# Optimization experiments

Measured on AMD Instinct MI355X. Metric: run time of the kernel, lower is better.

The kernel has to match this reference:

```python
import jax, jax.numpy as jnp
import numpy as np

# dims (match init_kwargs / input_specs)
B, T, IN, H, OUT, BR = 128, 250, 700, 512, 20, 4
VTH, DT, WARMUP = 1.0, 1.0, 10


@jax.custom_vjp
def spike_fn(v):
    # Heaviside spike with surrogate gradient (ActFun_adp style)
    return (v > 0.0).astype(v.dtype)

def _spike_fwd(v):
    return spike_fn(v), v

def _spike_bwd(v, g):
    gamma, lens = 0.5, 0.5  # gaussian surrogate
    return (g * gamma * jnp.exp(-v * v / (2.0 * lens * lens)),)

spike_fn.defvjp(_spike_fwd, _spike_bwd)


def make_mask(rng, out_dim, in_dim, branch):
    # each output neuron's branch j sees a disjoint random slice of inputs
    m = np.zeros((out_dim * branch, in_dim), np.float32)
    seg = in_dim // branch
    for i in range(out_dim):
        perm = rng.permutation(in_dim)
        for j in range(branch):
            m[i * branch + j, perm[j * seg:(j + 1) * seg]] = 1.0
    return jnp.asarray(m)


def setup_inputs() -> dict:
    key = jax.random.key(0)
    ks = jax.random.split(key, 12)
    rng = np.random.default_rng(0)
    lim1 = 1.0 / np.sqrt(IN)
    lim2 = 1.0 / np.sqrt(H)
    return {
        "x": jax.random.uniform(ks[0], (B, T, IN), dtype=jnp.float32),
        "W1": jax.random.uniform(ks[1], (H * BR, IN), minval=-lim1, maxval=lim1),
        "b1": jax.random.uniform(ks[2], (H * BR,), minval=-lim1, maxval=lim1),
        "tau_m1": jax.random.uniform(ks[3], (H,), minval=0.0, maxval=4.0),
        "tau_n1": jax.random.uniform(ks[4], (H, BR), minval=0.0, maxval=4.0),
        "mask1": make_mask(rng, H, IN, BR),
        "W2": jax.random.uniform(ks[5], (H * BR, H), minval=-lim2, maxval=lim2),
        "b2": jax.random.uniform(ks[6], (H * BR,), minval=-lim2, maxval=lim2),
        "tau_m2": jax.random.uniform(ks[7], (H,), minval=0.0, maxval=4.0),
        "tau_n2": jax.random.uniform(ks[8], (H, BR), minval=0.0, maxval=4.0),
        "mask2": make_mask(rng, H, H, BR),
        "Wo": jax.random.uniform(ks[9], (OUT, H), minval=-lim2, maxval=lim2),
        "bo": jax.random.uniform(ks[10], (OUT,), minval=-lim2, maxval=lim2),
        "tau_mo": jax.random.uniform(ks[11], (OUT,), minval=0.0, maxval=4.0),
    }


def reference(x, W1, b1, tau_m1, tau_n1, mask1, W2, b2, tau_m2, tau_n2, mask2, Wo, bo, tau_mo):
    beta1 = jax.nn.sigmoid(tau_n1)   # [H,BR] dendritic decay
    alpha1 = jax.nn.sigmoid(tau_m1)  # [H]   membrane decay
    beta2 = jax.nn.sigmoid(tau_n2)
    alpha2 = jax.nn.sigmoid(tau_m2)
    alpha_o = jax.nn.sigmoid(tau_mo)  # [OUT]
    Wm1 = W1 * mask1  # dendritic branch connectivity mask
    Wm2 = W2 * mask2
    Bsz = x.shape[0]
    Hd, Br = tau_n1.shape
    Od = tau_mo.shape[0]

    init = (jnp.zeros((Bsz, Hd, Br)), jnp.zeros((Bsz, Hd)), jnp.zeros((Bsz, Hd)),
            jnp.zeros((Bsz, Hd, Br)), jnp.zeros((Bsz, Hd)), jnp.zeros((Bsz, Hd)),
            jnp.zeros((Bsz, Od)))

    def step(c, xt):
        d1, m1, s1, d2, m2, s2, mo = c
        # layer 1: dendritic filter then LIF membrane with soft reset
        d1 = beta1 * d1 + (1.0 - beta1) * (xt @ Wm1.T + b1).reshape(Bsz, Hd, Br)
        m1 = m1 * alpha1 + (1.0 - alpha1) * DT * d1.sum(-1) - VTH * s1
        s1 = spike_fn(m1 - VTH)
        # layer 2
        d2 = beta2 * d2 + (1.0 - beta2) * (s1 @ Wm2.T + b2).reshape(Bsz, Hd, Br)
        m2 = m2 * alpha2 + (1.0 - alpha2) * DT * d2.sum(-1) - VTH * s2
        s2 = spike_fn(m2 - VTH)
        # leaky readout integrator (no spiking)
        mo = mo * alpha_o + (1.0 - alpha_o) * DT * (s2 @ Wo.T + bo)
        return (d1, m1, s1, d2, m2, s2, mo), jax.nn.softmax(mo, axis=1)

    _, ys = jax.lax.scan(step, init, jnp.swapaxes(x, 0, 1))  # ys: [T,B,OUT]
    # readout_mode == 'sum_softmax': skip steps i <= warmup_steps, sum the rest
    return ys[WARMUP + 1:].sum(0)
```

## Files before the change

kernel.cpp:

```cpp
#include <hip/hip_runtime.h>
#include <math.h>
#include <stdint.h>

#define B_    128
#define T_    250
#define IN_   700
#define INP_  704
#define H_    512
#define OUT_  20
#define BR_   4
#define HB_   2048
#define WARM_ 10
#define VTH_  1.0f

typedef __attribute__((ext_vector_type(8)))  _Float16 half8;
typedef __attribute__((ext_vector_type(4)))  float f32x4;
typedef __attribute__((ext_vector_type(16))) float f32x16;
typedef __attribute__((ext_vector_type(4)))  int i32x4;
typedef __attribute__((ext_vector_type(16))) int i32x16;
typedef const __attribute__((address_space(1))) void* gptr_t;
typedef __attribute__((address_space(3))) void* lptr_t;

__global__ __launch_bounds__(256)
void w1prep_kernel(const float* __restrict__ W, const float* __restrict__ M,
                   _Float16* __restrict__ w0, _Float16* __restrict__ w1) {
    int i = blockIdx.x * 256 + threadIdx.x;
    if (i >= HB_ * INP_) return;
    int r = i / INP_, c = i - r * INP_;
    float v = (c < IN_) ? W[(size_t)r * IN_ + c] * M[(size_t)r * IN_ + c] : 0.f;
    _Float16 h0 = (_Float16)v;
    w0[i] = h0;
    w1[i] = (_Float16)(v - (float)h0);
}

__global__ __launch_bounds__(256)
void w2prep_kernel(const float* __restrict__ W, const float* __restrict__ M,
                   int8_t* __restrict__ p2, int8_t* __restrict__ p1,
                   int8_t* __restrict__ p0) {
    int i = blockIdx.x * 256 + threadIdx.x;
    if (i >= HB_ * H_) return;
    float v = W[i] * M[i];
    int q = (int)lrintf(v * 67108864.f);
    int b0 = (int)(int8_t)(q & 0xFF);  q = (q - b0) >> 8;
    int b1 = (int)(int8_t)(q & 0xFF);  int b2 = (q - b1) >> 8;
    p0[i] = (int8_t)b0; p1[i] = (int8_t)b1; p2[i] = (int8_t)b2;
}

__global__ __launch_bounds__(256)
void woprep_kernel(const float* __restrict__ Wo, _Float16* __restrict__ wo0,
                   _Float16* __restrict__ wo1) {
    int i = blockIdx.x * 256 + threadIdx.x;
    if (i >= 32 * H_) return;
    int n = i >> 9;
    float v = (n < OUT_) ? Wo[(size_t)n * H_ + (i & (H_ - 1))] : 0.f;
    _Float16 h0 = (_Float16)v;
    wo0[i] = h0;
    wo1[i] = (_Float16)(v - (float)h0);
}

__global__ __launch_bounds__(256)
void convx_kernel(const float* __restrict__ x, _Float16* __restrict__ x0,
                  _Float16* __restrict__ x1, int t0, int tc, int ntot) {
    int i = blockIdx.x * 256 + threadIdx.x;
    if (i >= ntot) return;
    int r = i / INP_, c = i - r * INP_;
    int bb = r / tc, tl = r - bb * tc;
    float v = (c < IN_) ? x[((size_t)bb * T_ + t0 + tl) * IN_ + c] : 0.f;
    _Float16 h0 = (_Float16)v;
    x0[i] = h0;
    x1[i] = (_Float16)(v - (float)h0);
}

__global__ void zero_kernel(float* __restrict__ p, int n4) {
    int i = blockIdx.x * blockDim.x + threadIdx.x;
    if (i < n4) ((float4*)p)[i] = make_float4(0.f, 0.f, 0.f, 0.f);
}

__global__ __launch_bounds__(256)
void l1_gemm_kernel(const _Float16* __restrict__ x0, const _Float16* __restrict__ x1,
                    const _Float16* __restrict__ w0, const _Float16* __restrict__ w1,
                    const float* __restrict__ bias, float* __restrict__ C) {
    __shared__ alignas(16) _Float16 S[2 * 16384];
    const int tid  = threadIdx.x;
    const int wave = tid >> 6, lane = tid & 63;
    const int bm = blockIdx.y * 128, bn = blockIdx.x * 128;

    const int    srow  = tid >> 2;
    const int    skoff = (((tid & 3) ^ ((srow >> 1) & 3)) * 8);
    const size_t aoff0 = (size_t)(bm + srow) * INP_ + skoff;
    const size_t aoff1 = aoff0 + (size_t)64 * INP_;
    const size_t boff0 = (size_t)(bn + srow) * INP_ + skoff;
    const size_t boff1 = boff0 + (size_t)64 * INP_;
    const int lo = wave * 512;

    const int wm = wave & 1, wn = wave >> 1;
    const int row = lane & 31;
    const int khq = lane >> 5;
    const int key = (lane >> 1) & 3;
    const int cK0 = ((0 + khq) ^ key) * 8;
    const int cK1 = ((2 + khq) ^ key) * 8;

    f32x16 acc[2][2] = {};

    auto stage = [&](int kt, int base) {
        const int k0 = kt * 32;
        _Float16* Sb = S + base;
        __builtin_amdgcn_global_load_lds((gptr_t)(x0 + aoff0 + k0), (lptr_t)(Sb + lo),          16, 0, 0);
        __builtin_amdgcn_global_load_lds((gptr_t)(x0 + aoff1 + k0), (lptr_t)(Sb + 2048  + lo),  16, 0, 0);
        __builtin_amdgcn_global_load_lds((gptr_t)(x1 + aoff0 + k0), (lptr_t)(Sb + 4096  + lo),  16, 0, 0);
        __builtin_amdgcn_global_load_lds((gptr_t)(x1 + aoff1 + k0), (lptr_t)(Sb + 6144  + lo),  16, 0, 0);
        __builtin_amdgcn_global_load_lds((gptr_t)(w0 + boff0 + k0), (lptr_t)(Sb + 8192  + lo),  16, 0, 0);
        __builtin_amdgcn_global_load_lds((gptr_t)(w0 + boff1 + k0), (lptr_t)(Sb + 10240 + lo),  16, 0, 0);
        __builtin_amdgcn_global_load_lds((gptr_t)(w1 + boff0 + k0), (lptr_t)(Sb + 12288 + lo),  16, 0, 0);
        __builtin_amdgcn_global_load_lds((gptr_t)(w1 + boff1 + k0), (lptr_t)(Sb + 14336 + lo),  16, 0, 0);
    };

    auto compute = [&](int base) {
        const _Float16* A0b = S + base;
        const _Float16* A1b = A0b + 4096;
        const _Float16* B0b = A0b + 8192;
        const _Float16* B1b = A0b + 12288;
        half8 a0f[2][2], a1f[2][2], b0f[2][2], b1f[2][2];
#pragma unroll
        for (int mt = 0; mt < 2; mt++) {
            const _Float16* ar = &A0b[(wm * 64 + mt * 32 + row) * 32];
            a0f[mt][0] = *(const half8*)&ar[cK0];
            a0f[mt][1] = *(const half8*)&ar[cK1];
        }
#pragma unroll
        for (int nt = 0; nt < 2; nt++) {
            const _Float16* br = &B0b[(wn * 64 + nt * 32 + row) * 32];
            b0f[nt][0] = *(const half8*)&br[cK0];
            b0f[nt][1] = *(const half8*)&br[cK1];
        }
        __builtin_amdgcn_s_setprio(1);
#pragma unroll
        for (int ks = 0; ks < 2; ks++)
#pragma unroll
            for (int mt = 0; mt < 2; mt++)
#pragma unroll
                for (int nt = 0; nt < 2; nt++)
                    acc[mt][nt] = __builtin_amdgcn_mfma_f32_32x32x16_f16(
                        a0f[mt][ks], b0f[nt][ks], acc[mt][nt], 0, 0, 0);
        __builtin_amdgcn_s_setprio(0);
#pragma unroll
        for (int nt = 0; nt < 2; nt++) {
            const _Float16* br = &B1b[(wn * 64 + nt * 32 + row) * 32];
            b1f[nt][0] = *(const half8*)&br[cK0];
            b1f[nt][1] = *(const half8*)&br[cK1];
        }
        __builtin_amdgcn_s_setprio(1);
#pragma unroll
        for (int ks = 0; ks < 2; ks++)
#pragma unroll
            for (int mt = 0; mt < 2; mt++)
#pragma unroll
                for (int nt = 0; nt < 2; nt++)
                    acc[mt][nt] = __builtin_amdgcn_mfma_f32_32x32x16_f16(
                        a0f[mt][ks], b1f[nt][ks], acc[mt][nt], 0, 0, 0);
        __builtin_amdgcn_s_setprio(0);
#pragma unroll
        for (int mt = 0; mt < 2; mt++) {
            const _Float16* ar = &A1b[(wm * 64 + mt * 32 + row) * 32];
            a1f[mt][0] = *(const half8*)&ar[cK0];
            a1f[mt][1] = *(const half8*)&ar[cK1];
        }
        __builtin_amdgcn_s_setprio(1);
#pragma unroll
        for (int ks = 0; ks < 2; ks++)
#pragma unroll
            for (int mt = 0; mt < 2; mt++)
#pragma unroll
                for (int nt = 0; nt < 2; nt++)
                    acc[mt][nt] = __builtin_amdgcn_mfma_f32_32x32x16_f16(
                        a1f[mt][ks], b0f[nt][ks], acc[mt][nt], 0, 0, 0);
        __builtin_amdgcn_s_setprio(0);
    };

    stage(0, 0);
    asm volatile("s_waitcnt vmcnt(0)" ::: "memory");
    __builtin_amdgcn_s_barrier();

    int cur = 0;
    for (int kt = 0; kt < INP_ / 32 - 1; kt++) {
        const int base = cur * 16384;
        stage(kt + 1, base ^ 16384);
        compute(base);
        asm volatile("s_waitcnt vmcnt(0) lgkmcnt(0)" ::: "memory");
        __builtin_amdgcn_s_barrier();
        cur ^= 1;
    }
    compute(cur * 16384);

    const int col = lane & 31;
    const int rb  = 4 * (lane >> 5);
#pragma unroll
    for (int nt = 0; nt < 2; nt++) {
        const int gc = bn + wn * 64 + nt * 32 + col;
        const float bv = bias[gc];
#pragma unroll
        for (int mt = 0; mt < 2; mt++) {
#pragma unroll
            for (int reg = 0; reg < 16; reg++) {
                const int gr = bm + wm * 64 + mt * 32 + (reg & 3) + 8 * (reg >> 2) + rb;
                C[(size_t)gr * HB_ + gc] = acc[mt][nt][reg] + bv;
            }
        }
    }
}

__global__ __launch_bounds__(256)
void mfma_i8_gemm_kernel(const int8_t* __restrict__ A,
                         const int8_t* __restrict__ p2, const int8_t* __restrict__ p1,
                         const int8_t* __restrict__ p0,
                         const float* __restrict__ bias, float* __restrict__ C) {
    __shared__ alignas(16) int8_t S[2 * 16384];
    const int tid  = threadIdx.x;
    const int wave = tid >> 6, lane = tid & 63;
    const int bm = blockIdx.y * 128, bn = blockIdx.x * 128;

    const int    srow  = tid >> 2;
    const int    skoff = (((tid & 3) ^ ((srow >> 1) & 3)) * 16);
    const size_t aoff0 = (size_t)(bm + srow) * H_ + skoff;
    const size_t aoff1 = aoff0 + (size_t)64 * H_;
    const size_t boff0 = (size_t)(bn + srow) * H_ + skoff;
    const size_t boff1 = boff0 + (size_t)64 * H_;
    const int lo = wave * 1024;

    const int wm = wave & 1, wn = wave >> 1;
    const int row = lane & 31;
    const int khq = lane >> 5;
    const int key = (lane >> 1) & 3;
    const int cK0 = ((0 + khq) ^ key) * 16;
    const int cK1 = ((2 + khq) ^ key) * 16;

    i32x16 acc[2][2] = {};

    auto stage = [&](int i, int base) {
        const int s  = i >> 3;
        const int k0 = (i & 7) * 64;
        const int8_t* pw = (s == 0) ? p2 : (s == 1) ? p1 : p0;
        int8_t* Sb = S + base;
        __builtin_amdgcn_global_load_lds((gptr_t)(A  + aoff0 + k0), (lptr_t)(Sb + lo),          16, 0, 0);
        __builtin_amdgcn_global_load_lds((gptr_t)(A  + aoff1 + k0), (lptr_t)(Sb + 4096  + lo),  16, 0, 0);
        __builtin_amdgcn_global_load_lds((gptr_t)(pw + boff0 + k0), (lptr_t)(Sb + 8192  + lo),  16, 0, 0);
        __builtin_amdgcn_global_load_lds((gptr_t)(pw + boff1 + k0), (lptr_t)(Sb + 12288 + lo),  16, 0, 0);
    };

    auto compute = [&](int base) {
        const int8_t* Ab = S + base;
        const int8_t* Bb = Ab + 8192;
        i32x4 af[2][2], bf[2][2];
#pragma unroll
        for (int mt = 0; mt < 2; mt++) {
            const int8_t* ar = &Ab[(wm * 64 + mt * 32 + row) * 64];
            af[mt][0] = *(const i32x4*)&ar[cK0];
            af[mt][1] = *(const i32x4*)&ar[cK1];
        }
#pragma unroll
        for (int nt = 0; nt < 2; nt++) {
            const int8_t* br = &Bb[(wn * 64 + nt * 32 + row) * 64];
            bf[nt][0] = *(const i32x4*)&br[cK0];
            bf[nt][1] = *(const i32x4*)&br[cK1];
        }
        __builtin_amdgcn_s_setprio(1);
#pragma unroll
        for (int ks = 0; ks < 2; ks++)
#pragma unroll
            for (int mt = 0; mt < 2; mt++)
#pragma unroll
                for (int nt = 0; nt < 2; nt++)
                    acc[mt][nt] = __builtin_amdgcn_mfma_i32_32x32x32_i8(
                        af[mt][ks], bf[nt][ks], acc[mt][nt], 0, 0, 0);
        __builtin_amdgcn_s_setprio(0);
    };

    stage(0, 0);
    asm volatile("s_waitcnt vmcnt(0)" ::: "memory");
    __builtin_amdgcn_s_barrier();

    int cur = 0;
    for (int i = 0; i < 23; i++) {
        const int base = cur * 16384;
        stage(i + 1, base ^ 16384);
        if (i == 8 || i == 16) {
#pragma unroll
            for (int mt = 0; mt < 2; mt++)
#pragma unroll
                for (int nt = 0; nt < 2; nt++) acc[mt][nt] *= 256;
        }
        compute(base);
        asm volatile("s_waitcnt vmcnt(0) lgkmcnt(0)" ::: "memory");
        __builtin_amdgcn_s_barrier();
        cur ^= 1;
    }
    compute(cur * 16384);

    const float scale = 1.f / 67108864.f;
    const int col = lane & 31;
    const int rb  = 4 * (lane >> 5);
#pragma unroll
    for (int nt = 0; nt < 2; nt++) {
        const int gc = bn + wn * 64 + nt * 32 + col;
        const float bv = bias[gc];
#pragma unroll
        for (int mt = 0; mt < 2; mt++) {
#pragma unroll
            for (int reg = 0; reg < 16; reg++) {
                const int gr = bm + wm * 64 + mt * 32 + (reg & 3) + 8 * (reg >> 2) + rb;
                C[(size_t)gr * HB_ + gc] = (float)acc[mt][nt][reg] * scale + bv;
            }
        }
    }
}

#define SCAN_BODY(SPIKE_STORE)                                                  \
    int idx = blockIdx.x * 256 + threadIdx.x;                                   \
    int b = idx >> 9;                                                           \
    int h = idx & (H_ - 1);                                                     \
    float alpha = 1.f / (1.f + expf(-tau_m[h]));                                \
    float4 tn = ((const float4*)tau_n)[h];                                      \
    float4 beta;                                                                \
    beta.x = 1.f / (1.f + expf(-tn.x));                                         \
    beta.y = 1.f / (1.f + expf(-tn.y));                                         \
    beta.z = 1.f / (1.f + expf(-tn.z));                                         \
    beta.w = 1.f / (1.f + expf(-tn.w));                                         \
    float4 d = ((const float4*)dst)[idx];                                       \
    float m = mst[idx];                                                         \
    float sp = spst[idx];                                                       \
    const float* cp = cur + (size_t)b * tc * HB_ + h * BR_;                     \
    for (int t = 0; t < tc; t++) {                                              \
        float4 c = *(const float4*)cp;                                          \
        cp += HB_;                                                              \
        d.x = beta.x * d.x + (1.f - beta.x) * c.x;                              \
        d.y = beta.y * d.y + (1.f - beta.y) * c.y;                              \
        d.z = beta.z * d.z + (1.f - beta.z) * c.z;                              \
        d.w = beta.w * d.w + (1.f - beta.w) * c.w;                              \
        float s4 = ((d.x + d.y) + d.z) + d.w;                                   \
        m = m * alpha + (1.f - alpha) * s4 - VTH_ * sp;                         \
        sp = (m > VTH_) ? 1.f : 0.f;                                            \
        SPIKE_STORE;                                                            \
    }                                                                           \
    ((float4*)dst)[idx] = d;                                                    \
    mst[idx] = m;                                                               \
    spst[idx] = sp;

__global__ __launch_bounds__(256)
void scan_i8_kernel(const float* __restrict__ cur, float* __restrict__ dst,
                    float* __restrict__ mst, float* __restrict__ spst,
                    int8_t* __restrict__ sout, const float* __restrict__ tau_m,
                    const float* __restrict__ tau_n, int tc) {
    SCAN_BODY(sout[((size_t)b * tc + t) * H_ + h] = (int8_t)(m > VTH_))
}

__global__ __launch_bounds__(256)
void scan_f16_kernel(const float* __restrict__ cur, float* __restrict__ dst,
                     float* __restrict__ mst, float* __restrict__ spst,
                     _Float16* __restrict__ sout, const float* __restrict__ tau_m,
                     const float* __restrict__ tau_n, int tc) {
    SCAN_BODY(sout[((size_t)b * tc + t) * H_ + h] = (_Float16)sp)
}

__global__ __launch_bounds__(256)
void rdot_mfma_kernel(const _Float16* __restrict__ s2c, const _Float16* __restrict__ wo0,
                      const _Float16* __restrict__ wo1, const float* __restrict__ bo,
                      float* __restrict__ curo, int t0, int tc) {
    __shared__ alignas(16) _Float16 S[2 * 6144];
    const int tid  = threadIdx.x;
    const int wave = tid >> 6, lane = tid & 63;
    const int bm = blockIdx.x * 128;

    const int    srow  = tid >> 2;
    const int    skoff = (((tid & 3) ^ ((srow >> 1) & 3)) * 8);
    const size_t aoff0 = (size_t)(bm + srow) * H_ + skoff;
    const size_t aoff1 = aoff0 + (size_t)64 * H_;
    const _Float16* bsrc = (wave < 2) ? wo0 : wo1;
    const int bw = wave & 1;
    const size_t boff = (size_t)(bw * 16 + (lane >> 2)) * H_
                      + ((lane & 3) ^ ((lane >> 3) & 3)) * 8;
    const int loA = wave * 512;
    const int loB = 4096 + (wave >> 1) * 1024 + bw * 512;

    const int fr = lane & 15;
    const int key = (lane >> 1) & 3;
    const int cK  = (((lane >> 4) ^ key) * 8);

    f32x4 acc[2][2] = {};

    auto stage = [&](int kt, int base) {
        const int k0 = kt * 32;
        _Float16* Sb = S + base;
        __builtin_amdgcn_global_load_lds((gptr_t)(s2c + aoff0 + k0),  (lptr_t)(Sb + loA),        16, 0, 0);
        __builtin_amdgcn_global_load_lds((gptr_t)(s2c + aoff1 + k0),  (lptr_t)(Sb + 2048 + loA), 16, 0, 0);
        __builtin_amdgcn_global_load_lds((gptr_t)(bsrc + boff + k0),  (lptr_t)(Sb + loB),        16, 0, 0);
    };

    auto compute = [&](int base) {
        const _Float16* Ab  = S + base;
        const _Float16* B0b = Ab + 4096;
        const _Float16* B1b = Ab + 5120;
        half8 af[2], b0[2], b1[2];
#pragma unroll
        for (int mi = 0; mi < 2; mi++)
            af[mi] = *(const half8*)&Ab[(wave * 32 + mi * 16 + fr) * 32 + cK];
#pragma unroll
        for (int ni = 0; ni < 2; ni++) {
            b0[ni] = *(const half8*)&B0b[(ni * 16 + fr) * 32 + cK];
            b1[ni] = *(const half8*)&B1b[(ni * 16 + fr) * 32 + cK];
        }
        __builtin_amdgcn_s_setprio(1);
#pragma unroll
        for (int mi = 0; mi < 2; mi++)
#pragma unroll
            for (int ni = 0; ni < 2; ni++) {
                acc[mi][ni] = __builtin_amdgcn_mfma_f32_16x16x32_f16(af[mi], b0[ni], acc[mi][ni], 0, 0, 0);
                acc[mi][ni] = __builtin_amdgcn_mfma_f32_16x16x32_f16(af[mi], b1[ni], acc[mi][ni], 0, 0, 0);
            }
        __builtin_amdgcn_s_setprio(0);
    };

    stage(0, 0);
    asm volatile("s_waitcnt vmcnt(0)" ::: "memory");
    __builtin_amdgcn_s_barrier();

    int cur = 0;
    for (int kt = 0; kt < H_ / 32 - 1; kt++) {
        const int base = cur * 6144;
        stage(kt + 1, base ^ 6144);
        compute(base);
        asm volatile("s_waitcnt vmcnt(0) lgkmcnt(0)" ::: "memory");
        __builtin_amdgcn_s_barrier();
        cur ^= 1;
    }
    compute(cur * 6144);

    const int cc = lane & 15;
    const int cr = (lane >> 4) * 4;
#pragma unroll
    for (int ni = 0; ni < 2; ni++) {
        const int gc = ni * 16 + cc;
        if (gc < OUT_) {
            const float bv = bo[gc];
#pragma unroll
            for (int mi = 0; mi < 2; mi++) {
#pragma unroll
                for (int r = 0; r < 4; r++) {
                    const int gr = bm + wave * 32 + mi * 16 + cr + r;
                    const int bb = gr / tc, tl = gr - bb * tc;
                    curo[((size_t)bb * T_ + t0 + tl) * OUT_ + gc] = acc[mi][ni][r] + bv;
                }
            }
        }
    }
}

#define RT_SEG 12
#define RT_LEN 21

__global__ __launch_bounds__(256)
void readout_kernel(const float* __restrict__ curo, const float* __restrict__ tau_mo,
                    float* __restrict__ out) {
    __shared__ float moS[T_ * OUT_];
    __shared__ float segA[RT_SEG][OUT_];
    __shared__ float segU[RT_SEG][OUT_];
    __shared__ float pre[RT_SEG][OUT_];
    __shared__ float accS[OUT_];
    const int b = blockIdx.x;
    const int tid = threadIdx.x;
    const float* cb = curo + (size_t)b * T_ * OUT_;

    const int o = tid % OUT_;
    const int sg = tid / OUT_;
    const float ao = 1.f / (1.f + expf(-tau_mo[o]));

    if (tid < RT_SEG * OUT_) {
        int t0 = sg * RT_LEN;
        int t1 = min(T_, t0 + RT_LEN);
        float u = 0.f, Ap = 1.f;
        for (int t = t0; t < t1; t++) {
            u = ao * u + (1.f - ao) * cb[t * OUT_ + o];
            Ap *= ao;
        }
        segU[sg][o] = u; segA[sg][o] = Ap;
    }
    if (tid < OUT_) accS[tid] = 0.f;
    __syncthreads();
    if (tid < OUT_) {
        float m = 0.f;
        for (int s = 0; s < RT_SEG; s++) {
            pre[s][tid] = m;
            m = segA[s][tid] * m + segU[s][tid];
        }
    }
    __syncthreads();
    if (tid < RT_SEG * OUT_) {
        int t0 = sg * RT_LEN;
        int t1 = min(T_, t0 + RT_LEN);
        float m = pre[sg][o];
        for (int t = t0; t < t1; t++) {
            m = ao * m + (1.f - ao) * cb[t * OUT_ + o];
            moS[t * OUT_ + o] = m;
        }
    }
    __syncthreads();
    if (tid >= WARM_ + 1 && tid < T_) {
        int t = tid;
        float mx = -3.0e38f;
#pragma unroll
        for (int o2 = 0; o2 < OUT_; o2++) mx = fmaxf(mx, moS[t * OUT_ + o2]);
        float es[OUT_]; float se = 0.f;
#pragma unroll
        for (int o2 = 0; o2 < OUT_; o2++) {
            float e = expf(moS[t * OUT_ + o2] - mx);
            es[o2] = e; se += e;
        }
        float inv = 1.f / se;
#pragma unroll
        for (int o2 = 0; o2 < OUT_; o2++) atomicAdd(&accS[o2], es[o2] * inv);
    }
    __syncthreads();
    if (tid < OUT_) out[(size_t)b * OUT_ + tid] = accS[tid];
}

extern "C" void kernel_launch(void* const* d_in, const int* in_sizes, int n_in,
                              void* d_out, int out_size, void* d_ws, size_t ws_size,
                              hipStream_t stream) {
    const float* x      = (const float*)d_in[0];
    const float* W1     = (const float*)d_in[1];
    const float* b1     = (const float*)d_in[2];
    const float* tau_m1 = (const float*)d_in[3];
    const float* tau_n1 = (const float*)d_in[4];
    const float* mask1  = (const float*)d_in[5];
    const float* W2     = (const float*)d_in[6];
    const float* b2     = (const float*)d_in[7];
    const float* tau_m2 = (const float*)d_in[8];
    const float* tau_n2 = (const float*)d_in[9];
    const float* mask2  = (const float*)d_in[10];
    const float* Wo     = (const float*)d_in[11];
    const float* bo     = (const float*)d_in[12];
    const float* tau_mo = (const float*)d_in[13];
    float* out = (float*)d_out;

    int ncs;  int tcs[3];
    bool single = (ws_size >= (size_t)368000000);
    if (single)                                { ncs = 1; tcs[0] = 250; }
    else if (ws_size >= (size_t)219000000)     { ncs = 2; tcs[0] = tcs[1] = 125; }
    else                                       { ncs = 3; tcs[0] = 100; tcs[1] = 100; tcs[2] = 50; }
    const int tcm = tcs[0];

    char* p = (char*)d_ws;
    auto alloc = [&](size_t bytes) { char* r = p; p += (bytes + 255) & ~(size_t)255; return r; };
    _Float16* w10 = (_Float16*)alloc((size_t)HB_ * INP_ * 2);
    _Float16* w11 = (_Float16*)alloc((size_t)HB_ * INP_ * 2);
    int8_t*   q2  = (int8_t*)alloc((size_t)HB_ * H_);
    int8_t*   q1  = (int8_t*)alloc((size_t)HB_ * H_);
    int8_t*   q0  = (int8_t*)alloc((size_t)HB_ * H_);
    _Float16* wo0 = (_Float16*)alloc((size_t)32 * H_ * 2);
    _Float16* wo1 = (_Float16*)alloc((size_t)32 * H_ * 2);
    _Float16* xc0 = (_Float16*)alloc((size_t)B_ * tcm * INP_ * 2);
    _Float16* xc1 = (_Float16*)alloc((size_t)B_ * tcm * INP_ * 2);
    int8_t*   s1c;
    _Float16* s2c;
    if (single) {
        s1c = (int8_t*)xc0;
        s2c = (_Float16*)xc1;
    } else {
        s1c = (int8_t*)alloc((size_t)B_ * tcm * H_);
        s2c = (_Float16*)alloc((size_t)B_ * tcm * H_ * 2);
    }
    float* cur    = (float*)alloc((size_t)B_ * tcm * HB_ * 4);
    float* curo   = (float*)alloc((size_t)B_ * T_ * OUT_ * 4);
    float* st     = (float*)alloc((size_t)786432 * 4);
    float* d1  = st;
    float* m1  = d1 + (size_t)B_ * H_ * BR_;
    float* sp1 = m1 + (size_t)B_ * H_;
    float* d2  = sp1 + (size_t)B_ * H_;
    float* m2  = d2 + (size_t)B_ * H_ * BR_;
    float* sp2 = m2 + (size_t)B_ * H_;

    w1prep_kernel<<<(HB_ * INP_ + 255) / 256, 256, 0, stream>>>(W1, mask1, w10, w11);
    w2prep_kernel<<<(HB_ * H_ + 255) / 256, 256, 0, stream>>>(W2, mask2, q2, q1, q0);
    woprep_kernel<<<(32 * H_ + 255) / 256, 256, 0, stream>>>(Wo, wo0, wo1);
    zero_kernel<<<(786432 / 4 + 255) / 256, 256, 0, stream>>>(st, 786432 / 4);

    int t0 = 0;
    for (int c = 0; c < ncs; c++) {
        const int tc = tcs[c];
        const int M = B_ * tc;
        dim3 gg(HB_ / 128, M / 128);
        convx_kernel<<<(M * INP_ + 255) / 256, 256, 0, stream>>>(x, xc0, xc1, t0, tc, M * INP_);
        l1_gemm_kernel<<<gg, 256, 0, stream>>>(xc0, xc1, w10, w11, b1, cur);
        scan_i8_kernel<<<B_ * H_ / 256, 256, 0, stream>>>(cur, d1, m1, sp1, s1c, tau_m1, tau_n1, tc);
        mfma_i8_gemm_kernel<<<gg, 256, 0, stream>>>(s1c, q2, q1, q0, b2, cur);
        scan_f16_kernel<<<B_ * H_ / 256, 256, 0, stream>>>(cur, d2, m2, sp2, s2c, tau_m2, tau_n2, tc);
        rdot_mfma_kernel<<<M / 128, 256, 0, stream>>>(s2c, wo0, wo1, bo, curo, t0, tc);
        t0 += tc;
    }
    readout_kernel<<<B_, 256, 0, stream>>>(curo, tau_mo, out);
}
```

Baseline: 827.7 us.

## Load A operands directly to registers from pre-tiled x layout, remap workgroups

The x conversion kernel now writes x0/x1 in an MFMA-fragment-tiled layout, so the layer-1 GEMM can load A fragments straight from global memory into registers instead of staging them through LDS. LDS is halved to hold only the B (weight) tiles, and the k-loop is unrolled by two with register double-buffering and sched barriers, using partial vmcnt waits. Workgroup IDs are also remapped in an XCD-aware way. This cuts LDS traffic and footprint but adds register pressure, and it depends on other users of x0/x1 expecting the new layout.

```diff
diff --git a/kernel.cpp b/kernel.cpp
--- a/kernel.cpp
+++ b/kernel.cpp
@@ -21,6 +21,8 @@
 typedef const __attribute__((address_space(1))) void* gptr_t;
 typedef __attribute__((address_space(3))) void* lptr_t;
 
+#define SB0() __builtin_amdgcn_sched_barrier(0)
+
 __global__ __launch_bounds__(256)
 void w1prep_kernel(const float* __restrict__ W, const float* __restrict__ M,
                    _Float16* __restrict__ w0, _Float16* __restrict__ w1) {
@@ -67,8 +69,10 @@
     int bb = r / tc, tl = r - bb * tc;
     float v = (c < IN_) ? x[((size_t)bb * T_ + t0 + tl) * IN_ + c] : 0.f;
     _Float16 h0 = (_Float16)v;
-    x0[i] = h0;
-    x1[i] = (_Float16)(v - (float)h0);
+    size_t off = ((((size_t)(r >> 5) * 22 + (c >> 5)) * 4 + ((c >> 3) & 3)) * 32
+                  + (r & 31)) * 8 + (c & 7);
+    x0[off] = h0;
+    x1[off] = (_Float16)(v - (float)h0);
 }
 
 __global__ void zero_kernel(float* __restrict__ p, int n4) {
@@ -80,15 +84,18 @@
 void l1_gemm_kernel(const _Float16* __restrict__ x0, const _Float16* __restrict__ x1,
                     const _Float16* __restrict__ w0, const _Float16* __restrict__ w1,
                     const float* __restrict__ bias, float* __restrict__ C) {
-    __shared__ alignas(16) _Float16 S[2 * 16384];
+    __shared__ alignas(16) _Float16 S[2 * 8192];
     const int tid  = threadIdx.x;
     const int wave = tid >> 6, lane = tid & 63;
-    const int bm = blockIdx.y * 128, bn = blockIdx.x * 128;
+
+    const int nwg = (int)(gridDim.x * gridDim.y);
+    const int cpx = nwg >> 3;
+    const int id0 = (int)(blockIdx.y * gridDim.x + blockIdx.x);
+    const int id  = (id0 & 7) * cpx + (id0 >> 3);
+    const int bm = (id >> 4) * 128, bn = (id & 15) * 128;
 
     const int    srow  = tid >> 2;
     const int    skoff = (((tid & 3) ^ ((srow >> 1) & 3)) * 8);
-    const size_t aoff0 = (size_t)(bm + srow) * INP_ + skoff;
-    const size_t aoff1 = aoff0 + (size_t)64 * INP_;
     const size_t boff0 = (size_t)(bn + srow) * INP_ + skoff;
     const size_t boff1 = boff0 + (size_t)64 * INP_;
     const int lo = wave * 512;
@@ -100,38 +107,45 @@
     const int cK0 = ((0 + khq) ^ key) * 8;
     const int cK1 = ((2 + khq) ^ key) * 8;
 
+    const size_t mb0   = (size_t)(bm >> 5) + wm * 2;
+    const size_t aoffl = (size_t)(lane >> 5) * 256 + (size_t)(lane & 31) * 8;
+
     f32x16 acc[2][2] = {};
-
-    auto stage = [&](int kt, int base) {
+    half8 aP[2][2][2], aQ[2][2][2];
+
+    auto stageB = [&](int kt, int base) {
         const int k0 = kt * 32;
         _Float16* Sb = S + base;
-        __builtin_amdgcn_global_load_lds((gptr_t)(x0 + aoff0 + k0), (lptr_t)(Sb + lo),          16, 0, 0);
-        __builtin_amdgcn_global_load_lds((gptr_t)(x0 + aoff1 + k0), (lptr_t)(Sb + 2048  + lo),  16, 0, 0);
-        __builtin_amdgcn_global_load_lds((gptr_t)(x1 + aoff0 + k0), (lptr_t)(Sb + 4096  + lo),  16, 0, 0);
-        __builtin_amdgcn_global_load_lds((gptr_t)(x1 + aoff1 + k0), (lptr_t)(Sb + 6144  + lo),  16, 0, 0);
-        __builtin_amdgcn_global_load_lds((gptr_t)(w0 + boff0 + k0), (lptr_t)(Sb + 8192  + lo),  16, 0, 0);
-        __builtin_amdgcn_global_load_lds((gptr_t)(w0 + boff1 + k0), (lptr_t)(Sb + 10240 + lo),  16, 0, 0);
-        __builtin_amdgcn_global_load_lds((gptr_t)(w1 + boff0 + k0), (lptr_t)(Sb + 12288 + lo),  16, 0, 0);
-        __builtin_amdgcn_global_load_lds((gptr_t)(w1 + boff1 + k0), (lptr_t)(Sb + 14336 + lo),  16, 0, 0);
+        __builtin_amdgcn_global_load_lds((gptr_t)(w0 + boff0 + k0), (lptr_t)(Sb + lo),         16, 0, 0);
+        __builtin_amdgcn_global_load_lds((gptr_t)(w0 + boff1 + k0), (lptr_t)(Sb + 2048 + lo),  16, 0, 0);
+        __builtin_amdgcn_global_load_lds((gptr_t)(w1 + boff0 + k0), (lptr_t)(Sb + 4096 + lo),  16, 0, 0);
+        __builtin_amdgcn_global_load_lds((gptr_t)(w1 + boff1 + k0), (lptr_t)(Sb + 6144 + lo),  16, 0, 0);
     };
 
-    auto compute = [&](int base) {
-        const _Float16* A0b = S + base;
-        const _Float16* A1b = A0b + 4096;
-        const _Float16* B0b = A0b + 8192;
-        const _Float16* B1b = A0b + 12288;
-        half8 a0f[2][2], a1f[2][2], b0f[2][2], b1f[2][2];
+    auto loadA = [&](half8 (&d)[2][2][2], int kt) {
 #pragma unroll
         for (int mt = 0; mt < 2; mt++) {
-            const _Float16* ar = &A0b[(wm * 64 + mt * 32 + row) * 32];
-            a0f[mt][0] = *(const half8*)&ar[cK0];
-            a0f[mt][1] = *(const half8*)&ar[cK1];
-        }
+            const size_t rb = ((mb0 + mt) * 22 + kt) * 1024 + aoffl;
+#pragma unroll
+            for (int ks = 0; ks < 2; ks++) {
+                d[0][mt][ks] = *(const half8*)(x0 + rb + ks * 512);
+                d[1][mt][ks] = *(const half8*)(x1 + rb + ks * 512);
+            }
+        }
+    };
+
+    auto comp = [&](const half8 (&a)[2][2][2], int base) {
+        const _Float16* B0b = S + base;
+        const _Float16* B1b = S + base + 4096;
+        half8 b0f[2][2], b1f[2][2];
 #pragma unroll
         for (int nt = 0; nt < 2; nt++) {
-            const _Float16* br = &B0b[(wn * 64 + nt * 32 + row) * 32];
-            b0f[nt][0] = *(const half8*)&br[cK0];
-            b0f[nt][1] = *(const half8*)&br[cK1];
+            const _Float16* br0 = &B0b[(wn * 64 + nt * 32 + row) * 32];
+            b0f[nt][0] = *(const half8*)&br0[cK0];
+            b0f[nt][1] = *(const half8*)&br0[cK1];
+            const _Float16* br1 = &B1b[(wn * 64 + nt * 32 + row) * 32];
+            b1f[nt][0] = *(const half8*)&br1[cK0];
+            b1f[nt][1] = *(const half8*)&br1[cK1];
         }
         __builtin_amdgcn_s_setprio(1);
 #pragma unroll
@@ -141,15 +155,7 @@
 #pragma unroll
                 for (int nt = 0; nt < 2; nt++)
                     acc[mt][nt] = __builtin_amdgcn_mfma_f32_32x32x16_f16(
-                        a0f[mt][ks], b0f[nt][ks], acc[mt][nt], 0, 0, 0);
-        __builtin_amdgcn_s_setprio(0);
-#pragma unroll
-        for (int nt = 0; nt < 2; nt++) {
-            const _Float16* br = &B1b[(wn * 64 + nt * 32 + row) * 32];
-            b1f[nt][0] = *(const half8*)&br[cK0];
-            b1f[nt][1] = *(const half8*)&br[cK1];
-        }
-        __builtin_amdgcn_s_setprio(1);
+                        a[0][mt][ks], b0f[nt][ks], acc[mt][nt], 0, 0, 0);
 #pragma unroll
         for (int ks = 0; ks < 2; ks++)
 #pragma unroll
@@ -157,15 +163,7 @@
 #pragma unroll
                 for (int nt = 0; nt < 2; nt++)
                     acc[mt][nt] = __builtin_amdgcn_mfma_f32_32x32x16_f16(
-                        a0f[mt][ks], b1f[nt][ks], acc[mt][nt], 0, 0, 0);
-        __builtin_amdgcn_s_setprio(0);
-#pragma unroll
-        for (int mt = 0; mt < 2; mt++) {
-            const _Float16* ar = &A1b[(wm * 64 + mt * 32 + row) * 32];
-            a1f[mt][0] = *(const half8*)&ar[cK0];
-            a1f[mt][1] = *(const half8*)&ar[cK1];
-        }
-        __builtin_amdgcn_s_setprio(1);
+                        a[0][mt][ks], b1f[nt][ks], acc[mt][nt], 0, 0, 0);
 #pragma unroll
         for (int ks = 0; ks < 2; ks++)
 #pragma unroll
@@ -173,24 +171,34 @@
 #pragma unroll
                 for (int nt = 0; nt < 2; nt++)
                     acc[mt][nt] = __builtin_amdgcn_mfma_f32_32x32x16_f16(
-                        a1f[mt][ks], b0f[nt][ks], acc[mt][nt], 0, 0, 0);
+                        a[1][mt][ks], b0f[nt][ks], acc[mt][nt], 0, 0, 0);
         __builtin_amdgcn_s_setprio(0);
     };
 
-    stage(0, 0);
+    stageB(0, 0);
+    SB0();
+    loadA(aP, 0);
+    SB0();
     asm volatile("s_waitcnt vmcnt(0)" ::: "memory");
     __builtin_amdgcn_s_barrier();
 
-    int cur = 0;
-    for (int kt = 0; kt < INP_ / 32 - 1; kt++) {
-        const int base = cur * 16384;
-        stage(kt + 1, base ^ 16384);
-        compute(base);
-        asm volatile("s_waitcnt vmcnt(0) lgkmcnt(0)" ::: "memory");
+#pragma unroll 1
+    for (int it = 0; it < 10; it++) {
+        const int kt = it * 2;
+        stageB(kt + 1, 8192); SB0(); loadA(aQ, kt + 1); SB0();
+        comp(aP, 0);
+        asm volatile("s_waitcnt vmcnt(8) lgkmcnt(0)" ::: "memory"); SB0();
         __builtin_amdgcn_s_barrier();
-        cur ^= 1;
-    }
-    compute(cur * 16384);
+        stageB(kt + 2, 0); SB0(); loadA(aP, kt + 2); SB0();
+        comp(aQ, 8192);
+        asm volatile("s_waitcnt vmcnt(8) lgkmcnt(0)" ::: "memory"); SB0();
+        __builtin_amdgcn_s_barrier();
+    }
+    stageB(21, 8192); SB0(); loadA(aQ, 21); SB0();
+    comp(aP, 0);
+    asm volatile("s_waitcnt vmcnt(8) lgkmcnt(0)" ::: "memory"); SB0();
+    __builtin_amdgcn_s_barrier();
+    comp(aQ, 8192);
 
     const int col = lane & 31;
     const int rb  = 4 * (lane >> 5);
```

Measured after the change: 878.2 us. +6.1%, slower.

## Fuse per-batch time scans into GEMM epilogues with padded 128-step tiles

Applied to the files above, without the earlier changes.

Each GEMM block now covers one batch element's 125 timesteps, padded to 128, and 128 current columns (32 neurons). The block stages its tile of currents in LDS, and 32 threads run the dendritic/LIF recurrence over time right there. This removes the fp32 current buffer round trip through global memory and the separate scan kernels. In exchange, the serial scan runs on only 32 threads per block while the other waves idle, LDS use rises to about 70KB, which limits occupancy, and 3 of every 128 rows are padding work.

```diff
diff --git a/kernel.cpp b/kernel.cpp
--- a/kernel.cpp
+++ b/kernel.cpp
@@ -12,6 +12,9 @@
 #define HB_   2048
 #define WARM_ 10
 #define VTH_  1.0f
+#define TC_   125
+#define TP_   128
+#define MP_   16384
 
 typedef __attribute__((ext_vector_type(8)))  _Float16 half8;
 typedef __attribute__((ext_vector_type(4)))  float f32x4;
@@ -60,12 +63,12 @@
 
 __global__ __launch_bounds__(256)
 void convx_kernel(const float* __restrict__ x, _Float16* __restrict__ x0,
-                  _Float16* __restrict__ x1, int t0, int tc, int ntot) {
+                  _Float16* __restrict__ x1, int t0) {
     int i = blockIdx.x * 256 + threadIdx.x;
-    if (i >= ntot) return;
+    if (i >= MP_ * INP_) return;
     int r = i / INP_, c = i - r * INP_;
-    int bb = r / tc, tl = r - bb * tc;
-    float v = (c < IN_) ? x[((size_t)bb * T_ + t0 + tl) * IN_ + c] : 0.f;
+    int bb = r >> 7, tl = r & (TP_ - 1);
+    float v = (tl < TC_ && c < IN_) ? x[((size_t)bb * T_ + t0 + tl) * IN_ + c] : 0.f;
     _Float16 h0 = (_Float16)v;
     x0[i] = h0;
     x1[i] = (_Float16)(v - (float)h0);
@@ -77,13 +80,21 @@
 }
 
 __global__ __launch_bounds__(256)
-void l1_gemm_kernel(const _Float16* __restrict__ x0, const _Float16* __restrict__ x1,
-                    const _Float16* __restrict__ w0, const _Float16* __restrict__ w1,
-                    const float* __restrict__ bias, float* __restrict__ C) {
-    __shared__ alignas(16) _Float16 S[2 * 16384];
+void l1_fused_kernel(const _Float16* __restrict__ x0, const _Float16* __restrict__ x1,
+                     const _Float16* __restrict__ w0, const _Float16* __restrict__ w1,
+                     const float* __restrict__ bias,
+                     float* __restrict__ dst, float* __restrict__ mst,
+                     float* __restrict__ spst, int8_t* __restrict__ sout,
+                     const float* __restrict__ tau_m, const float* __restrict__ tau_n) {
+    __shared__ alignas(16) char SMEM[69632];
+    _Float16* S    = (_Float16*)SMEM;
+    float*    curS = (float*)SMEM;
+    int8_t*   sbuf = (int8_t*)(SMEM + 65536);
+
     const int tid  = threadIdx.x;
     const int wave = tid >> 6, lane = tid & 63;
-    const int bm = blockIdx.y * 128, bn = blockIdx.x * 128;
+    const int bb = blockIdx.y;
+    const int bm = bb * TP_, bn = blockIdx.x * 128;
 
     const int    srow  = tid >> 2;
     const int    skoff = (((tid & 3) ^ ((srow >> 1) & 3)) * 8);
@@ -191,33 +202,80 @@
         cur ^= 1;
     }
     compute(cur * 16384);
+    __syncthreads();
 
     const int col = lane & 31;
     const int rb  = 4 * (lane >> 5);
 #pragma unroll
     for (int nt = 0; nt < 2; nt++) {
-        const int gc = bn + wn * 64 + nt * 32 + col;
-        const float bv = bias[gc];
+        const int lcol = wn * 64 + nt * 32 + col;
+        const float bv = bias[bn + lcol];
 #pragma unroll
         for (int mt = 0; mt < 2; mt++) {
 #pragma unroll
             for (int reg = 0; reg < 16; reg++) {
-                const int gr = bm + wm * 64 + mt * 32 + (reg & 3) + 8 * (reg >> 2) + rb;
-                C[(size_t)gr * HB_ + gc] = acc[mt][nt][reg] + bv;
+                const int trow = wm * 64 + mt * 32 + (reg & 3) + 8 * (reg >> 2) + rb;
+                curS[trow * 128 + lcol] = acc[mt][nt][reg] + bv;
             }
         }
     }
-}
-
-__global__ __launch_bounds__(256)
-void mfma_i8_gemm_kernel(const int8_t* __restrict__ A,
-                         const int8_t* __restrict__ p2, const int8_t* __restrict__ p1,
-                         const int8_t* __restrict__ p0,
-                         const float* __restrict__ bias, float* __restrict__ C) {
-    __shared__ alignas(16) int8_t S[2 * 16384];
+    __syncthreads();
+
+    if (tid < 32) {
+        const int hg   = blockIdx.x * 32 + tid;
+        const int sidx = bb * H_ + hg;
+        float alpha = 1.f / (1.f + expf(-tau_m[hg]));
+        float4 tn = ((const float4*)tau_n)[hg];
+        float4 beta;
+        beta.x = 1.f / (1.f + expf(-tn.x));
+        beta.y = 1.f / (1.f + expf(-tn.y));
+        beta.z = 1.f / (1.f + expf(-tn.z));
+        beta.w = 1.f / (1.f + expf(-tn.w));
+        float4 d = ((const float4*)dst)[sidx];
+        float m = mst[sidx];
+        float sp = spst[sidx];
+#pragma unroll 5
+        for (int t = 0; t < TC_; t++) {
+            float4 c = ((const float4*)(curS + t * 128))[tid];
+            d.x = beta.x * d.x + (1.f - beta.x) * c.x;
+            d.y = beta.y * d.y + (1.f - beta.y) * c.y;
+            d.z = beta.z * d.z + (1.f - beta.z) * c.z;
+            d.w = beta.w * d.w + (1.f - beta.w) * c.w;
+            float s4 = ((d.x + d.y) + d.z) + d.w;
+            m = m * alpha + (1.f - alpha) * s4 - VTH_ * sp;
+            sp = (m > VTH_) ? 1.f : 0.f;
+            sbuf[t * 32 + tid] = (int8_t)(m > VTH_);
+        }
+        sbuf[125 * 32 + tid] = 0; sbuf[126 * 32 + tid] = 0; sbuf[127 * 32 + tid] = 0;
+        ((float4*)dst)[sidx] = d;
+        mst[sidx] = m;
+        spst[sidx] = sp;
+    }
+    __syncthreads();
+    if (tid < TP_) {
+        int4* dp = (int4*)&sout[((size_t)(bm + tid)) * H_ + blockIdx.x * 32];
+        const int4* sp4 = (const int4*)&sbuf[tid * 32];
+        dp[0] = sp4[0]; dp[1] = sp4[1];
+    }
+}
+
+__global__ __launch_bounds__(256)
+void l2_fused_kernel(const int8_t* __restrict__ A,
+                     const int8_t* __restrict__ p2, const int8_t* __restrict__ p1,
+                     const int8_t* __restrict__ p0,
+                     const float* __restrict__ bias,
+                     float* __restrict__ dst, float* __restrict__ mst,
+                     float* __restrict__ spst, _Float16* __restrict__ sout,
+                     const float* __restrict__ tau_m, const float* __restrict__ tau_n) {
+    __shared__ alignas(16) char SMEM[73728];
+    int8_t*   S    = (int8_t*)SMEM;
+    float*    curS = (float*)SMEM;
+    _Float16* sbuf = (_Float16*)(SMEM + 65536);
+
     const int tid  = threadIdx.x;
     const int wave = tid >> 6, lane = tid & 63;
-    const int bm = blockIdx.y * 128, bn = blockIdx.x * 128;
+    const int bb = blockIdx.y;
+    const int bm = bb * TP_, bn = blockIdx.x * 128;
 
     const int    srow  = tid >> 2;
     const int    skoff = (((tid & 3) ^ ((srow >> 1) & 3)) * 16);
@@ -295,76 +353,70 @@
         cur ^= 1;
     }
     compute(cur * 16384);
+    __syncthreads();
 
     const float scale = 1.f / 67108864.f;
     const int col = lane & 31;
     const int rb  = 4 * (lane >> 5);
 #pragma unroll
     for (int nt = 0; nt < 2; nt++) {
-        const int gc = bn + wn * 64 + nt * 32 + col;
-        const float bv = bias[gc];
+        const int lcol = wn * 64 + nt * 32 + col;
+        const float bv = bias[bn + lcol];
 #pragma unroll
         for (int mt = 0; mt < 2; mt++) {
 #pragma unroll
             for (int reg = 0; reg < 16; reg++) {
-                const int gr = bm + wm * 64 + mt * 32 + (reg & 3) + 8 * (reg >> 2) + rb;
-                C[(size_t)gr * HB_ + gc] = (float)acc[mt][nt][reg] * scale + bv;
+                const int trow = wm * 64 + mt * 32 + (reg & 3) + 8 * (reg >> 2) + rb;
+                curS[trow * 128 + lcol] = (float)acc[mt][nt][reg] * scale + bv;
             }
         }
     }
-}
-
-#define SCAN_BODY(SPIKE_STORE)                                                  \
-    int idx = blockIdx.x * 256 + threadIdx.x;                                   \
-    int b = idx >> 9;                                                           \
-    int h = idx & (H_ - 1);                                                     \
-    float alpha = 1.f / (1.f + expf(-tau_m[h]));                                \
-    float4 tn = ((const float4*)tau_n)[h];                                      \
-    float4 beta;                                                                \
-    beta.x = 1.f / (1.f + expf(-tn.x));                                         \
-    beta.y = 1.f / (1.f + expf(-tn.y));                                         \
-    beta.z = 1.f / (1.f + expf(-tn.z));                                         \
-    beta.w = 1.f / (1.f + expf(-tn.w));                                         \
-    float4 d = ((const float4*)dst)[idx];                                       \
-    float m = mst[idx];                                                         \
-    float sp = spst[idx];                                                       \
-    const float* cp = cur + (size_t)b * tc * HB_ + h * BR_;                     \
-    for (int t = 0; t < tc; t++) {                                              \
-        float4 c = *(const float4*)cp;                                          \
-        cp += HB_;                                                              \
-        d.x = beta.x * d.x + (1.f - beta.x) * c.x;                              \
-        d.y = beta.y * d.y + (1.f - beta.y) * c.y;                              \
-        d.z = beta.z * d.z + (1.f - beta.z) * c.z;                              \
-        d.w = beta.w * d.w + (1.f - beta.w) * c.w;                              \
-        float s4 = ((d.x + d.y) + d.z) + d.w;                                   \
-        m = m * alpha + (1.f - alpha) * s4 - VTH_ * sp;                         \
-        sp = (m > VTH_) ? 1.f : 0.f;                                            \
-        SPIKE_STORE;                                                            \
-    }                                                                           \
-    ((float4*)dst)[idx] = d;                                                    \
-    mst[idx] = m;                                                               \
-    spst[idx] = sp;
-
-__global__ __launch_bounds__(256)
-void scan_i8_kernel(const float* __restrict__ cur, float* __restrict__ dst,
-                    float* __restrict__ mst, float* __restrict__ spst,
-                    int8_t* __restrict__ sout, const float* __restrict__ tau_m,
-                    const float* __restrict__ tau_n, int tc) {
-    SCAN_BODY(sout[((size_t)b * tc + t) * H_ + h] = (int8_t)(m > VTH_))
-}
-
-__global__ __launch_bounds__(256)
-void scan_f16_kernel(const float* __restrict__ cur, float* __restrict__ dst,
-                     float* __restrict__ mst, float* __restrict__ spst,
-                     _Float16* __restrict__ sout, const float* __restrict__ tau_m,
-                     const float* __restrict__ tau_n, int tc) {
-    SCAN_BODY(sout[((size_t)b * tc + t) * H_ + h] = (_Float16)sp)
+    __syncthreads();
+
+    if (tid < 32) {
+        const int hg   = blockIdx.x * 32 + tid;
+        const int sidx = bb * H_ + hg;
+        float alpha = 1.f / (1.f + expf(-tau_m[hg]));
+        float4 tn = ((const float4*)tau_n)[hg];
+        float4 beta;
+        beta.x = 1.f / (1.f + expf(-tn.x));
+        beta.y = 1.f / (1.f + expf(-tn.y));
+        beta.z = 1.f / (1.f + expf(-tn.z));
+        beta.w = 1.f / (1.f + expf(-tn.w));
+        float4 d = ((const float4*)dst)[sidx];
+        float m = mst[sidx];
+        float sp = spst[sidx];
+#pragma unroll 5
+        for (int t = 0; t < TC_; t++) {
+            float4 c = ((const float4*)(curS + t * 128))[tid];
+            d.x = beta.x * d.x + (1.f - beta.x) * c.x;
+            d.y = beta.y * d.y + (1.f - beta.y) * c.y;
+            d.z = beta.z * d.z + (1.f - beta.z) * c.z;
+            d.w = beta.w * d.w + (1.f - beta.w) * c.w;
+            float s4 = ((d.x + d.y) + d.z) + d.w;
+            m = m * alpha + (1.f - alpha) * s4 - VTH_ * sp;
+            sp = (m > VTH_) ? 1.f : 0.f;
+            sbuf[t * 32 + tid] = (_Float16)sp;
+        }
+        sbuf[125 * 32 + tid] = (_Float16)0.f;
+        sbuf[126 * 32 + tid] = (_Float16)0.f;
+        sbuf[127 * 32 + tid] = (_Float16)0.f;
+        ((float4*)dst)[sidx] = d;
+        mst[sidx] = m;
+        spst[sidx] = sp;
+    }
+    __syncthreads();
+    if (tid < TP_) {
+        int4* dp = (int4*)&sout[((size_t)(bm + tid)) * H_ + blockIdx.x * 32];
+        const int4* sp4 = (const int4*)&sbuf[tid * 32];
+        dp[0] = sp4[0]; dp[1] = sp4[1]; dp[2] = sp4[2]; dp[3] = sp4[3];
+    }
 }
 
 __global__ __launch_bounds__(256)
 void rdot_mfma_kernel(const _Float16* __restrict__ s2c, const _Float16* __restrict__ wo0,
                       const _Float16* __restrict__ wo1, const float* __restrict__ bo,
-                      float* __restrict__ curo, int t0, int tc) {
+                      float* __restrict__ curo, int t0) {
     __shared__ alignas(16) _Float16 S[2 * 6144];
     const int tid  = threadIdx.x;
     const int wave = tid >> 6, lane = tid & 63;
@@ -446,8 +498,9 @@
 #pragma unroll
                 for (int r = 0; r < 4; r++) {
                     const int gr = bm + wave * 32 + mi * 16 + cr + r;
-                    const int bb = gr / tc, tl = gr - bb * tc;
-                    curo[((size_t)bb * T_ + t0 + tl) * OUT_ + gc] = acc[mi][ni][r] + bv;
+                    const int bb = gr >> 7, tl = gr & (TP_ - 1);
+                    if (tl < TC_)
+                        curo[((size_t)bb * T_ + t0 + tl) * OUT_ + gc] = acc[mi][ni][r] + bv;
                 }
             }
         }
@@ -541,13 +594,6 @@
     const float* tau_mo = (const float*)d_in[13];
     float* out = (float*)d_out;
 
-    int ncs;  int tcs[3];
-    bool single = (ws_size >= (size_t)368000000);
-    if (single)                                { ncs = 1; tcs[0] = 250; }
-    else if (ws_size >= (size_t)219000000)     { ncs = 2; tcs[0] = tcs[1] = 125; }
-    else                                       { ncs = 3; tcs[0] = 100; tcs[1] = 100; tcs[2] = 50; }
-    const int tcm = tcs[0];
-
     char* p = (char*)d_ws;
     auto alloc = [&](size_t bytes) { char* r = p; p += (bytes + 255) & ~(size_t)255; return r; };
     _Float16* w10 = (_Float16*)alloc((size_t)HB_ * INP_ * 2);
@@ -557,18 +603,10 @@
     int8_t*   q0  = (int8_t*)alloc((size_t)HB_ * H_);
     _Float16* wo0 = (_Float16*)alloc((size_t)32 * H_ * 2);
     _Float16* wo1 = (_Float16*)alloc((size_t)32 * H_ * 2);
-    _Float16* xc0 = (_Float16*)alloc((size_t)B_ * tcm * INP_ * 2);
-    _Float16* xc1 = (_Float16*)alloc((size_t)B_ * tcm * INP_ * 2);
-    int8_t*   s1c;
-    _Float16* s2c;
-    if (single) {
-        s1c = (int8_t*)xc0;
-        s2c = (_Float16*)xc1;
-    } else {
-        s1c = (int8_t*)alloc((size_t)B_ * tcm * H_);
-        s2c = (_Float16*)alloc((size_t)B_ * tcm * H_ * 2);
-    }
-    float* cur    = (float*)alloc((size_t)B_ * tcm * HB_ * 4);
+    _Float16* xc0 = (_Float16*)alloc((size_t)MP_ * INP_ * 2);
+    _Float16* xc1 = (_Float16*)alloc((size_t)MP_ * INP_ * 2);
+    int8_t*   s1c = (int8_t*)alloc((size_t)MP_ * H_);
+    _Float16* s2c = (_Float16*)alloc((size_t)MP_ * H_ * 2);
     float* curo   = (float*)alloc((size_t)B_ * T_ * OUT_ * 4);
     float* st     = (float*)alloc((size_t)786432 * 4);
     float* d1  = st;
@@ -583,18 +621,15 @@
     woprep_kernel<<<(32 * H_ + 255) / 256, 256, 0, stream>>>(Wo, wo0, wo1);
     zero_kernel<<<(786432 / 4 + 255) / 256, 256, 0, stream>>>(st, 786432 / 4);
 
-    int t0 = 0;
-    for (int c = 0; c < ncs; c++) {
-        const int tc = tcs[c];
-        const int M = B_ * tc;
-        dim3 gg(HB_ / 128, M / 128);
-        convx_kernel<<<(M * INP_ + 255) / 256, 256, 0, stream>>>(x, xc0, xc1, t0, tc, M * INP_);
-        l1_gemm_kernel<<<gg, 256, 0, stream>>>(xc0, xc1, w10, w11, b1, cur);
-        scan_i8_kernel<<<B_ * H_ / 256, 256, 0, stream>>>(cur, d1, m1, sp1, s1c, tau_m1, tau_n1, tc);
-        mfma_i8_gemm_kernel<<<gg, 256, 0, stream>>>(s1c, q2, q1, q0, b2, cur);
-        scan_f16_kernel<<<B_ * H_ / 256, 256, 0, stream>>>(cur, d2, m2, sp2, s2c, tau_m2, tau_n2, tc);
-        rdot_mfma_kernel<<<M / 128, 256, 0, stream>>>(s2c, wo0, wo1, bo, curo, t0, tc);
-        t0 += tc;
+    dim3 gg(HB_ / 128, B_);
+    for (int c = 0; c < 2; c++) {
+        const int t0 = c * TC_;
+        convx_kernel<<<(MP_ * INP_) / 256, 256, 0, stream>>>(x, xc0, xc1, t0);
+        l1_fused_kernel<<<gg, 256, 0, stream>>>(xc0, xc1, w10, w11, b1,
+                                                d1, m1, sp1, s1c, tau_m1, tau_n1);
+        l2_fused_kernel<<<gg, 256, 0, stream>>>(s1c, q2, q1, q0, b2,
+                                                d2, m2, sp2, s2c, tau_m2, tau_n2);
+        rdot_mfma_kernel<<<MP_ / 128, 256, 0, stream>>>(s2c, wo0, wo1, bo, curo, t0);
     }
     readout_kernel<<<B_, 256, 0, stream>>>(curo, tau_mo, out);
 }
```

Result: faster. 785.3 us, median of 2 (-5.1%).
